# Kernel tuning notes

Measured on AMD Instinct MI355X. Metric: run time of the kernel, lower is better.

The kernel has to match this reference:

```python
import jax, jax.numpy as jnp
import numpy as np

HEAD_DIM = 64

def setup_inputs() -> dict:
    key = jax.random.key(0)
    kq, kk, kv = jax.random.split(key, 3)
    shape = (2, 4096, 8, HEAD_DIM)  # [B, S, H, D]
    q = jax.random.normal(kq, shape, dtype=jnp.float32)
    k = jax.random.normal(kk, shape, dtype=jnp.float32)
    v = jax.random.normal(kv, shape, dtype=jnp.float32)
    return {"q": q, "k": k, "v": v}

def reference(q, k, v):
    # Single-process path of SimpleRingAttention: standard softmax attention.
    # q,k,v: [B, S, H, D]; scores computed per head.
    scale = 1.0 / jnp.sqrt(jnp.asarray(HEAD_DIM, dtype=q.dtype))
    scores = jnp.einsum('bqhd,bkhd->bhqk', q, k) * scale  # [B,H,S,S]
    attn = jax.nn.softmax(scores, axis=-1)
    out = jnp.einsum('bhqk,bkhd->bqhd', attn, v)  # back to [B,S,H,D]
    return out
```

## Files before the change

kernel.cpp:

```cpp
#include <hip/hip_runtime.h>
#include <hip/hip_bf16.h>

#define B_ 2
#define S_ 4096
#define H_ 8
#define D_ 64
#define BQ 128
#define BK 64

#define GLOBAL_AS __attribute__((address_space(1)))
#define LDS_AS    __attribute__((address_space(3)))

typedef short bf16x8 __attribute__((ext_vector_type(8)));
typedef short bf16x4 __attribute__((ext_vector_type(4)));
typedef float f32x4  __attribute__((ext_vector_type(4)));

#define QSCALE 0.18033688011112043f

__device__ __forceinline__ short f2bf(float f) {
    __bf16 h = (__bf16)f;
    return __builtin_bit_cast(short, h);
}

__device__ __forceinline__ bf16x8 pack8(float4 f0, float4 f1) {
    bf16x8 r;
    r[0]=f2bf(f0.x); r[1]=f2bf(f0.y); r[2]=f2bf(f0.z); r[3]=f2bf(f0.w);
    r[4]=f2bf(f1.x); r[5]=f2bf(f1.y); r[6]=f2bf(f1.z); r[7]=f2bf(f1.w);
    return r;
}

__device__ __forceinline__ bf16x8 pack8s(float4 f0, float4 f1, float s) {
    bf16x8 r;
    r[0]=f2bf(f0.x*s); r[1]=f2bf(f0.y*s); r[2]=f2bf(f0.z*s); r[3]=f2bf(f0.w*s);
    r[4]=f2bf(f1.x*s); r[5]=f2bf(f1.y*s); r[6]=f2bf(f1.z*s); r[7]=f2bf(f1.w*s);
    return r;
}

__global__ __launch_bounds__(256) void cast_kv_kernel(
    const float* __restrict__ kin, const float* __restrict__ vin,
    unsigned short* __restrict__ kb, unsigned short* __restrict__ vtb)
{
    __shared__ float Lf[64][72];
    const int role = blockIdx.z & 1;
    const int b    = blockIdx.z >> 1;
    const int h    = blockIdx.y;
    const int s0   = blockIdx.x * 64;
    const int t    = threadIdx.x;

    if (role == 0) {
        int r = t >> 2, fq = t & 3;
        const float4* gp = (const float4*)(kin + (((size_t)(b*S_ + s0 + r)*H_ + h)*D_ + fq*16));
        bf16x8 o0 = pack8(gp[0], gp[1]);
        bf16x8 o1 = pack8(gp[2], gp[3]);
        unsigned short* ob = kb + ((size_t)(b*H_ + h)*S_ + s0 + r)*D_ + fq*16;
        *(bf16x8*)ob       = o0;
        *(bf16x8*)(ob + 8) = o1;
    } else {
        {
            int r  = t >> 2, fq = t & 3;
            const float4* gp = (const float4*)(vin + (((size_t)(b*S_ + s0 + r)*H_ + h)*D_ + fq*16));
            #pragma unroll
            for (int j = 0; j < 4; ++j)
                *(f32x4*)&Lf[r][fq*16 + 4*j] = (f32x4){gp[j].x, gp[j].y, gp[j].z, gp[j].w};
        }
        __syncthreads();
        {
            int d = t >> 2, sq = t & 3;
            bf16x8 o0, o1;
            #pragma unroll
            for (int j = 0; j < 8; ++j) o0[j] = f2bf(Lf[sq*16 + j][d]);
            #pragma unroll
            for (int j = 0; j < 8; ++j) o1[j] = f2bf(Lf[sq*16 + 8 + j][d]);
            unsigned short* ob = vtb + (((size_t)(b*H_ + h)*D_ + d)*S_ + s0 + sq*16);
            *(bf16x8*)(ob)     = o0;
            *(bf16x8*)(ob + 8) = o1;
        }
    }
}

template<bool SPLIT>
__global__ __launch_bounds__(256, 4) void fattn_kernel(
    const float* __restrict__ q, const unsigned short* __restrict__ kb,
    const unsigned short* __restrict__ vtb, float* __restrict__ out,
    float* __restrict__ Op, float* __restrict__ lw)
{
    __shared__ unsigned short Ks [BK][64];
    __shared__ unsigned short Vts[D_][64];
    __shared__ unsigned short Ps [BQ][64];

    const int tid  = threadIdx.x;
    const int wave = tid >> 6;
    const int lane = tid & 63;
    const int m16  = tid & 15;
    const int quad = (tid & 63) >> 4;
    const int h    = blockIdx.y;
    const int b    = SPLIT ? (blockIdx.z >> 1) : blockIdx.z;
    const int half = SPLIT ? (blockIdx.z & 1)  : 0;
    const int kt0  = half * 32;
    const int nkt  = SPLIT ? 32 : 64;
    const int q0   = blockIdx.x * BQ;
    const int bS   = b * S_;
    const int wq2  = wave * 32;
    const int r7   = m16 & 7;

    int ksoff[2][4];
    #pragma unroll
    for (int kh = 0; kh < 2; ++kh)
        #pragma unroll
        for (int t4 = 0; t4 < 4; ++t4)
            ksoff[kh][t4] = (t4*16 + m16)*64 + (((kh*4 + quad) ^ r7)*8);
    int proff[2][2];
    #pragma unroll
    for (int n = 0; n < 2; ++n)
        #pragma unroll
        for (int kh = 0; kh < 2; ++kh)
            proff[n][kh] = (wq2 + n*16 + m16)*64 + (((kh*4 + quad) ^ r7)*8);
    int pwoff[2][4];
    #pragma unroll
    for (int n = 0; n < 2; ++n)
        #pragma unroll
        for (int mt = 0; mt < 4; ++mt)
            pwoff[n][mt] = (wq2 + n*16 + m16)*64
                         + (((2*mt + (quad>>1)) ^ r7)*8) + (quad&1)*4;

    const int srow = (lane >> 3);
    const int c8g  = (lane & 7) ^ srow;
    const int wqs  = wave * 16;
    const unsigned short* ksg[2];
    const unsigned short* vtg[2];
    #pragma unroll
    for (int it = 0; it < 2; ++it) {
        int rk = wqs + it*8 + srow;
        ksg[it] = kb  + ((size_t)(b*H_ + h)*S_ + rk)*64 + c8g*8;
        vtg[it] = vtb + ((size_t)(b*H_ + h)*D_ + rk)*(size_t)S_ + c8g*8;
    }

    bf16x8 bq[2][2];
    #pragma unroll
    for (int n = 0; n < 2; ++n) {
        const int qrow = q0 + wq2 + n*16 + m16;
        const float* qp = q + ((size_t)(bS + qrow)*H_ + h)*D_;
        #pragma unroll
        for (int kh = 0; kh < 2; ++kh) {
            const float4* q4 = (const float4*)(qp + kh*32 + quad*8);
            bq[n][kh] = pack8s(q4[0], q4[1], QSCALE);
        }
    }

    const short ONE = 0x3F80;
    bf16x8 ones = { ONE,ONE,ONE,ONE,ONE,ONE,ONE,ONE };

    f32x4 oacc[2][4];
    f32x4 lacc[2];
    #pragma unroll
    for (int n = 0; n < 2; ++n) {
        lacc[n] = (f32x4){0.f,0.f,0.f,0.f};
        #pragma unroll
        for (int dt = 0; dt < 4; ++dt) oacc[n][dt] = (f32x4){0.f,0.f,0.f,0.f};
    }

    for (int i = 0; i < nkt; ++i) {
        const int kt = kt0 + i;
        __syncthreads();

        #pragma unroll
        for (int it = 0; it < 2; ++it) {
            __builtin_amdgcn_global_load_lds(
                (const GLOBAL_AS void*)(ksg[it] + (size_t)kt*BK*64),
                (LDS_AS void*)&Ks[wqs + it*8][0], 16, 0, 0);
            __builtin_amdgcn_global_load_lds(
                (const GLOBAL_AS void*)(vtg[it] + (size_t)kt*BK),
                (LDS_AS void*)&Vts[wqs + it*8][0], 16, 0, 0);
        }
        __syncthreads();

        #pragma unroll
        for (int mt = 0; mt < 4; ++mt) {
            f32x4 s0 = (f32x4){0.f,0.f,0.f,0.f};
            f32x4 s1 = (f32x4){0.f,0.f,0.f,0.f};
            #pragma unroll
            for (int kh = 0; kh < 2; ++kh) {
                bf16x8 aK = *(const bf16x8*)&Ks[0][ksoff[kh][mt]];
                s0 = __builtin_amdgcn_mfma_f32_16x16x32_bf16(aK, bq[0][kh], s0, 0,0,0);
                s1 = __builtin_amdgcn_mfma_f32_16x16x32_bf16(aK, bq[1][kh], s1, 0,0,0);
            }
            bf16x4 p0, p1;
            #pragma unroll
            for (int r = 0; r < 4; ++r) {
                p0[r] = f2bf(__builtin_exp2f(s0[r]));
                p1[r] = f2bf(__builtin_exp2f(s1[r]));
            }
            *(bf16x4*)&Ps[0][pwoff[0][mt]] = p0;
            *(bf16x4*)&Ps[0][pwoff[1][mt]] = p1;
        }

        #pragma unroll
        for (int kh = 0; kh < 2; ++kh) {
            bf16x8 bp0 = *(const bf16x8*)&Ps[0][proff[0][kh]];
            bf16x8 bp1 = *(const bf16x8*)&Ps[0][proff[1][kh]];
            lacc[0] = __builtin_amdgcn_mfma_f32_16x16x32_bf16(ones, bp0, lacc[0], 0,0,0);
            lacc[1] = __builtin_amdgcn_mfma_f32_16x16x32_bf16(ones, bp1, lacc[1], 0,0,0);
            #pragma unroll
            for (int dt = 0; dt < 4; ++dt) {
                bf16x8 aV = *(const bf16x8*)&Vts[0][ksoff[kh][dt]];
                oacc[0][dt] = __builtin_amdgcn_mfma_f32_16x16x32_bf16(aV, bp0, oacc[0][dt], 0,0,0);
                oacc[1][dt] = __builtin_amdgcn_mfma_f32_16x16x32_bf16(aV, bp1, oacc[1][dt], 0,0,0);
            }
        }
    }

    #pragma unroll
    for (int n = 0; n < 2; ++n) {
        const int orow = q0 + wq2 + n*16 + m16;
        if constexpr (SPLIT) {
            float* ob = Op + (size_t)half*((size_t)B_*S_*H_*D_)
                           + ((size_t)(bS + orow)*H_ + h)*D_;
            #pragma unroll
            for (int dt = 0; dt < 4; ++dt) {
                float4 o4 = { oacc[n][dt][0], oacc[n][dt][1],
                              oacc[n][dt][2], oacc[n][dt][3] };
                *(float4*)(ob + dt*16 + quad*4) = o4;
            }
            if (quad == 0)
                lw[(size_t)half*((size_t)B_*S_*H_) + (size_t)(bS + orow)*H_ + h] = lacc[n][0];
        } else {
            const float linv = 1.0f / lacc[n][0];
            float* ob = out + ((size_t)(bS + orow)*H_ + h)*D_;
            #pragma unroll
            for (int dt = 0; dt < 4; ++dt) {
                float4 o4 = { oacc[n][dt][0]*linv, oacc[n][dt][1]*linv,
                              oacc[n][dt][2]*linv, oacc[n][dt][3]*linv };
                *(float4*)(ob + dt*16 + quad*4) = o4;
            }
        }
    }
}

__global__ __launch_bounds__(256) void combine_kernel(
    const float* __restrict__ Op, const float* __restrict__ lw,
    float* __restrict__ out)
{
    const size_t NR = (size_t)B_*S_*H_;
    const size_t NO = NR * D_;
    const int t = threadIdx.x;
    size_t r  = (size_t)blockIdx.x * 16 + (t >> 4);
    int   c4  = t & 15;
    const float4* p0 = (const float4*)(Op + r*D_) + c4;
    const float4* p1 = (const float4*)(Op + NO + r*D_) + c4;
    float linv = 1.0f / (lw[r] + lw[NR + r]);
    float4 a = *p0, b = *p1;
    float4 o = { (a.x+b.x)*linv, (a.y+b.y)*linv, (a.z+b.z)*linv, (a.w+b.w)*linv };
    *((float4*)(out + r*D_) + c4) = o;
}

#define FBQ 64
#define LDK 72
__global__ __launch_bounds__(256, 4) void fattn_fb(
    const float* __restrict__ q, const float* __restrict__ k,
    const float* __restrict__ v, float* __restrict__ out)
{
    __shared__ unsigned short Ks [BK][LDK];
    __shared__ unsigned short Vts[D_][LDK];
    __shared__ unsigned short Ps [FBQ][LDK];
    const int tid  = threadIdx.x;
    const int wave = tid >> 6;
    const int m16  = tid & 15;
    const int quad = (tid & 63) >> 4;
    const int h    = blockIdx.y;
    const int b    = blockIdx.z;
    const int q0   = blockIdx.x * FBQ;
    const int bS   = b * S_;
    const int wq   = wave * 16;
    bf16x8 bq[2];
    {
        const int qrow = q0 + wq + m16;
        const float* qb = q + ((size_t)(bS + qrow)*H_ + h)*D_;
        #pragma unroll
        for (int kh = 0; kh < 2; ++kh) {
            const float4* qp = (const float4*)(qb + kh*32 + quad*8);
            bq[kh] = pack8s(qp[0], qp[1], QSCALE);
        }
    }
    const short ONE = 0x3F80;
    bf16x8 ones = { ONE,ONE,ONE,ONE,ONE,ONE,ONE,ONE };
    f32x4 oacc[4];
    f32x4 lacc = (f32x4){0.f,0.f,0.f,0.f};
    #pragma unroll
    for (int dt = 0; dt < 4; ++dt) oacc[dt] = (f32x4){0.f,0.f,0.f,0.f};
    const int vd  = tid & 63;
    const int vkg = tid >> 6;
    for (int kt = 0; kt < S_/BK; ++kt) {
        const int k0 = kt * BK;
        __syncthreads();
        #pragma unroll
        for (int i = 0; i < 2; ++i) {
            int chunk = tid + i*256;
            int row = chunk >> 3, c8 = chunk & 7;
            const float4* gp = (const float4*)(k + ((size_t)(bS + k0 + row)*H_ + h)*D_ + c8*8);
            *(bf16x8*)&Ks[row][c8*8] = pack8(gp[0], gp[1]);
        }
        {
            const float* vb = v + ((size_t)(bS + k0 + vkg*16)*H_ + h)*D_ + vd;
            bf16x8 t0, t1;
            #pragma unroll
            for (int i = 0; i < 8; ++i) t0[i] = f2bf(vb[(size_t)i * (H_*D_)]);
            #pragma unroll
            for (int i = 0; i < 8; ++i) t1[i] = f2bf(vb[(size_t)(i+8) * (H_*D_)]);
            *(bf16x8*)&Vts[vd][vkg*16]     = t0;
            *(bf16x8*)&Vts[vd][vkg*16 + 8] = t1;
        }
        __syncthreads();
        f32x4 sacc[4];
        #pragma unroll
        for (int mt = 0; mt < 4; ++mt) sacc[mt] = (f32x4){0.f,0.f,0.f,0.f};
        #pragma unroll
        for (int kh = 0; kh < 2; ++kh)
            #pragma unroll
            for (int mt = 0; mt < 4; ++mt) {
                bf16x8 aK = *(const bf16x8*)&Ks[mt*16 + m16][kh*32 + quad*8];
                sacc[mt] = __builtin_amdgcn_mfma_f32_16x16x32_bf16(aK, bq[kh], sacc[mt], 0,0,0);
            }
        #pragma unroll
        for (int mt = 0; mt < 4; ++mt) {
            bf16x4 pk;
            #pragma unroll
            for (int r = 0; r < 4; ++r)
                pk[r] = f2bf(__builtin_exp2f(sacc[mt][r]));
            *(bf16x4*)&Ps[wq + m16][mt*16 + quad*4] = pk;
        }
        #pragma unroll
        for (int kh = 0; kh < 2; ++kh) {
            bf16x8 bp = *(const bf16x8*)&Ps[wq + m16][kh*32 + quad*8];
            lacc = __builtin_amdgcn_mfma_f32_16x16x32_bf16(ones, bp, lacc, 0,0,0);
            #pragma unroll
            for (int dt = 0; dt < 4; ++dt) {
                bf16x8 aV = *(const bf16x8*)&Vts[dt*16 + m16][kh*32 + quad*8];
                oacc[dt] = __builtin_amdgcn_mfma_f32_16x16x32_bf16(aV, bp, oacc[dt], 0,0,0);
            }
        }
    }
    const float linv = 1.0f / lacc[0];
    const int orow = q0 + wq + m16;
    float* ob = out + ((size_t)(bS + orow)*H_ + h)*D_;
    #pragma unroll
    for (int dt = 0; dt < 4; ++dt) {
        float4 o4 = { oacc[dt][0]*linv, oacc[dt][1]*linv,
                      oacc[dt][2]*linv, oacc[dt][3]*linv };
        *(float4*)(ob + dt*16 + quad*4) = o4;
    }
}

extern "C" void kernel_launch(void* const* d_in, const int* in_sizes, int n_in,
                              void* d_out, int out_size, void* d_ws, size_t ws_size,
                              hipStream_t stream) {
    const float* q = (const float*)d_in[0];
    const float* k = (const float*)d_in[1];
    const float* v = (const float*)d_in[2];
    float* out = (float*)d_out;
    const size_t elems = (size_t)B_*H_*S_*D_;
    const size_t NR    = (size_t)B_*S_*H_;
    const size_t need_cast  = 2 * elems * sizeof(unsigned short);
    const size_t need_split = need_cast + 2*elems*sizeof(float) + 2*NR*sizeof(float);

    if (ws_size >= need_split) {
        unsigned short* kb  = (unsigned short*)d_ws;
        unsigned short* vtb = kb + elems;
        float* Op = (float*)(vtb + elems);
        float* lw = Op + 2*elems;
        cast_kv_kernel<<<dim3(S_/64, H_, B_*2), dim3(256), 0, stream>>>(k, v, kb, vtb);
        fattn_kernel<true><<<dim3(S_/BQ, H_, B_*2), dim3(256), 0, stream>>>(
            q, kb, vtb, out, Op, lw);
        combine_kernel<<<dim3((int)(NR/16)), dim3(256), 0, stream>>>(Op, lw, out);
    } else if (ws_size >= need_cast) {
        unsigned short* kb  = (unsigned short*)d_ws;
        unsigned short* vtb = kb + elems;
        cast_kv_kernel<<<dim3(S_/64, H_, B_*2), dim3(256), 0, stream>>>(k, v, kb, vtb);
        fattn_kernel<false><<<dim3(S_/BQ, H_, B_), dim3(256), 0, stream>>>(
            q, kb, vtb, out, nullptr, nullptr);
    } else {
        fattn_fb<<<dim3(S_/FBQ, H_, B_), dim3(256), 0, stream>>>(q, k, v, out);
    }
}
```

Before: 197.0 us.

## Double-buffer K tiles and split P/V stage into two half chunks

K tiles are now double-buffered in LDS. The next K tile is prefetched with global_load_lds while the current one is consumed, and the V tile load moves to the start of the iteration. The QK/softmax/PV work is split into two 32-column chunks, so the P scratch buffer shrinks to a padded 36-wide row, and the mid-iteration barrier is placed after the first chunk's P writes. The aim is to hide global load latency behind MFMA work and to cut LDS footprint. The cost is the loss of the XOR swizzle on P, which may cause some LDS bank conflicts.

Measured after the change: 200.2 us. About the same (+1.6%).

```diff
diff --git a/kernel.cpp b/kernel.cpp
--- a/kernel.cpp
+++ b/kernel.cpp
@@ -7,6 +7,7 @@
 #define D_ 64
 #define BQ 128
 #define BK 64
+#define PSW 36
 
 #define GLOBAL_AS __attribute__((address_space(1)))
 #define LDS_AS    __attribute__((address_space(3)))
@@ -84,9 +85,9 @@
     const unsigned short* __restrict__ vtb, float* __restrict__ out,
     float* __restrict__ Op, float* __restrict__ lw)
 {
-    __shared__ unsigned short Ks [BK][64];
+    __shared__ unsigned short Ksb[2][BK][64];
     __shared__ unsigned short Vts[D_][64];
-    __shared__ unsigned short Ps [BQ][64];
+    __shared__ unsigned short Ps [BQ][PSW];
 
     const int tid  = threadIdx.x;
     const int wave = tid >> 6;
@@ -109,19 +110,17 @@
         #pragma unroll
         for (int t4 = 0; t4 < 4; ++t4)
             ksoff[kh][t4] = (t4*16 + m16)*64 + (((kh*4 + quad) ^ r7)*8);
-    int proff[2][2];
-    #pragma unroll
-    for (int n = 0; n < 2; ++n)
-        #pragma unroll
-        for (int kh = 0; kh < 2; ++kh)
-            proff[n][kh] = (wq2 + n*16 + m16)*64 + (((kh*4 + quad) ^ r7)*8);
-    int pwoff[2][4];
-    #pragma unroll
-    for (int n = 0; n < 2; ++n)
-        #pragma unroll
-        for (int mt = 0; mt < 4; ++mt)
-            pwoff[n][mt] = (wq2 + n*16 + m16)*64
-                         + (((2*mt + (quad>>1)) ^ r7)*8) + (quad&1)*4;
+
+    int pwoff[2][2];
+    int proff[2];
+    #pragma unroll
+    for (int n = 0; n < 2; ++n) {
+        const int row = wq2 + n*16 + m16;
+        #pragma unroll
+        for (int mtl = 0; mtl < 2; ++mtl)
+            pwoff[n][mtl] = row*PSW + mtl*16 + quad*4;
+        proff[n] = row*PSW + quad*8;
+    }
 
     const int srow = (lane >> 3);
     const int c8g  = (lane & 7) ^ srow;
@@ -159,54 +158,68 @@
         for (int dt = 0; dt < 4; ++dt) oacc[n][dt] = (f32x4){0.f,0.f,0.f,0.f};
     }
 
+    #pragma unroll
+    for (int it = 0; it < 2; ++it)
+        __builtin_amdgcn_global_load_lds(
+            (const GLOBAL_AS void*)(ksg[it] + (size_t)kt0*BK*64),
+            (LDS_AS void*)&Ksb[0][wqs + it*8][0], 16, 0, 0);
+    __syncthreads();
+
     for (int i = 0; i < nkt; ++i) {
-        const int kt = kt0 + i;
-        __syncthreads();
-
-        #pragma unroll
-        for (int it = 0; it < 2; ++it) {
-            __builtin_amdgcn_global_load_lds(
-                (const GLOBAL_AS void*)(ksg[it] + (size_t)kt*BK*64),
-                (LDS_AS void*)&Ks[wqs + it*8][0], 16, 0, 0);
+        const int kt  = kt0 + i;
+        const int cur = i & 1;
+        const unsigned short* Kc = &Ksb[cur][0][0];
+
+        #pragma unroll
+        for (int it = 0; it < 2; ++it)
             __builtin_amdgcn_global_load_lds(
                 (const GLOBAL_AS void*)(vtg[it] + (size_t)kt*BK),
                 (LDS_AS void*)&Vts[wqs + it*8][0], 16, 0, 0);
-        }
-        __syncthreads();
-
-        #pragma unroll
-        for (int mt = 0; mt < 4; ++mt) {
-            f32x4 s0 = (f32x4){0.f,0.f,0.f,0.f};
-            f32x4 s1 = (f32x4){0.f,0.f,0.f,0.f};
-            #pragma unroll
-            for (int kh = 0; kh < 2; ++kh) {
-                bf16x8 aK = *(const bf16x8*)&Ks[0][ksoff[kh][mt]];
-                s0 = __builtin_amdgcn_mfma_f32_16x16x32_bf16(aK, bq[0][kh], s0, 0,0,0);
-                s1 = __builtin_amdgcn_mfma_f32_16x16x32_bf16(aK, bq[1][kh], s1, 0,0,0);
-            }
-            bf16x4 p0, p1;
-            #pragma unroll
-            for (int r = 0; r < 4; ++r) {
-                p0[r] = f2bf(__builtin_exp2f(s0[r]));
-                p1[r] = f2bf(__builtin_exp2f(s1[r]));
-            }
-            *(bf16x4*)&Ps[0][pwoff[0][mt]] = p0;
-            *(bf16x4*)&Ps[0][pwoff[1][mt]] = p1;
-        }
-
-        #pragma unroll
-        for (int kh = 0; kh < 2; ++kh) {
-            bf16x8 bp0 = *(const bf16x8*)&Ps[0][proff[0][kh]];
-            bf16x8 bp1 = *(const bf16x8*)&Ps[0][proff[1][kh]];
+        if (i + 1 < nkt) {
+            #pragma unroll
+            for (int it = 0; it < 2; ++it)
+                __builtin_amdgcn_global_load_lds(
+                    (const GLOBAL_AS void*)(ksg[it] + (size_t)(kt+1)*BK*64),
+                    (LDS_AS void*)&Ksb[cur^1][wqs + it*8][0], 16, 0, 0);
+        }
+
+        #pragma unroll
+        for (int c = 0; c < 2; ++c) {
+            #pragma unroll
+            for (int mtl = 0; mtl < 2; ++mtl) {
+                const int mt = c*2 + mtl;
+                f32x4 s0 = (f32x4){0.f,0.f,0.f,0.f};
+                f32x4 s1 = (f32x4){0.f,0.f,0.f,0.f};
+                #pragma unroll
+                for (int kh = 0; kh < 2; ++kh) {
+                    bf16x8 aK = *(const bf16x8*)&Kc[ksoff[kh][mt]];
+                    s0 = __builtin_amdgcn_mfma_f32_16x16x32_bf16(aK, bq[0][kh], s0, 0,0,0);
+                    s1 = __builtin_amdgcn_mfma_f32_16x16x32_bf16(aK, bq[1][kh], s1, 0,0,0);
+                }
+                bf16x4 p0, p1;
+                #pragma unroll
+                for (int r = 0; r < 4; ++r) {
+                    p0[r] = f2bf(__builtin_exp2f(s0[r]));
+                    p1[r] = f2bf(__builtin_exp2f(s1[r]));
+                }
+                *(bf16x4*)&Ps[0][pwoff[0][mtl]] = p0;
+                *(bf16x4*)&Ps[0][pwoff[1][mtl]] = p1;
+            }
+
+            if (c == 0) __syncthreads();
+
+            bf16x8 bp0 = *(const bf16x8*)&Ps[0][proff[0]];
+            bf16x8 bp1 = *(const bf16x8*)&Ps[0][proff[1]];
             lacc[0] = __builtin_amdgcn_mfma_f32_16x16x32_bf16(ones, bp0, lacc[0], 0,0,0);
             lacc[1] = __builtin_amdgcn_mfma_f32_16x16x32_bf16(ones, bp1, lacc[1], 0,0,0);
             #pragma unroll
             for (int dt = 0; dt < 4; ++dt) {
-                bf16x8 aV = *(const bf16x8*)&Vts[0][ksoff[kh][dt]];
+                bf16x8 aV = *(const bf16x8*)&Vts[0][ksoff[c][dt]];
                 oacc[0][dt] = __builtin_amdgcn_mfma_f32_16x16x32_bf16(aV, bp0, oacc[0][dt], 0,0,0);
                 oacc[1][dt] = __builtin_amdgcn_mfma_f32_16x16x32_bf16(aV, bp1, oacc[1][dt], 0,0,0);
             }
         }
+        __syncthreads();
     }
 
     #pragma unroll
```
